# Kernel tuning notes

Hardware: AMD Instinct MI355X
Metric: run time of the kernel (lower is better)

The kernel has to match this reference:

```python
import jax, jax.numpy as jnp
import numpy as np

N = 100000
E = 1600000
IN_C, HID_C, OUT_C = 128, 128, 64


def setup_inputs() -> dict:
    key = jax.random.key(0)
    k = jax.random.split(key, 8)
    x = jax.random.normal(k[0], (N, IN_C), dtype=jnp.float32)
    edge_index = jax.random.randint(k[1], (2, E), 0, N, dtype=jnp.int64)
    edge_attr = jax.random.uniform(k[2], (E,), dtype=jnp.float32)
    # Glorot-ish init for GCNConv weights, zero bias (PyG default)
    W1 = jax.random.normal(k[3], (IN_C, HID_C), dtype=jnp.float32) / np.sqrt(IN_C)
    b1 = jnp.zeros((HID_C,), dtype=jnp.float32)
    W2 = jax.random.normal(k[4], (HID_C, OUT_C), dtype=jnp.float32) / np.sqrt(HID_C)
    b2 = jnp.zeros((OUT_C,), dtype=jnp.float32)
    return {"x": x, "edge_index": edge_index, "edge_attr": edge_attr,
            "W1": W1, "b1": b1, "W2": W2, "b2": b2}


def _gcn_conv(x, W, b, src, dst, ew):
    """PyG GCNConv: add self-loops (weight 1), symmetric normalization,
    aggregate x@W over edges src->dst, add bias."""
    n = x.shape[0]
    loop = jnp.arange(n, dtype=src.dtype)
    src_f = jnp.concatenate([src, loop])            # [E+N]
    dst_f = jnp.concatenate([dst, loop])
    ew_f = jnp.concatenate([ew, jnp.ones((n,), dtype=ew.dtype)])
    deg = jax.ops.segment_sum(ew_f, dst_f, num_segments=n)  # [N]
    dis = jnp.where(deg > 0, jax.lax.rsqrt(jnp.maximum(deg, 1e-12)), 0.0)
    norm = dis[src_f] * ew_f * dis[dst_f]           # [E+N]
    h = x @ W                                       # [N, C_out]
    msg = norm[:, None] * h[src_f]                  # [E+N, C_out] gather
    out = jax.ops.segment_sum(msg, dst_f, num_segments=n)   # scatter-add
    return out + b


def reference(x, edge_index, edge_attr, W1, b1, W2, b2):
    src, dst = edge_index[0], edge_index[1]
    h = _gcn_conv(x, W1, b1, src, dst, edge_attr)
    h = jax.nn.relu(h)
    # dropout is identity in eval mode (training=False)
    out = _gcn_conv(h, W2, b2, src, dst, edge_attr)
    return out
```

## Files before the change

### kernel.cpp

```cpp
#include <hip/hip_runtime.h>

#define NN 100000
#define EE 1600000
#define NBKT 391
#define NCHK 391
#define BINCHUNK 4096
#define CAP 5120

typedef unsigned int uint;
typedef unsigned short ushort;
typedef unsigned long long u64;

__device__ inline ushort f2bf(float f) {
    uint u = __float_as_uint(f);
    return (ushort)((u + 0x7fffu + ((u >> 16) & 1u)) >> 16);
}
__device__ inline float bf_lo(uint u) { return __uint_as_float(u << 16); }
__device__ inline float bf_hi(uint u) { return __uint_as_float(u & 0xffff0000u); }

__global__ __launch_bounds__(256) void k_count(const int* __restrict__ dst,
                                               int* __restrict__ gcount) {
    __shared__ int bh[NBKT];
    int t = threadIdx.x;
    for (int i = t; i < NBKT; i += 256) bh[i] = 0;
    __syncthreads();
    int base = blockIdx.x * BINCHUNK;
    int lim = min(EE - base, BINCHUNK);
    for (int i = t; i < lim; i += 256) atomicAdd(&bh[dst[base + i] >> 8], 1);
    __syncthreads();
    for (int i = t; i < NBKT; i += 256)
        if (bh[i]) atomicAdd(&gcount[i], bh[i]);
}

__global__ __launch_bounds__(512) void k_bscan(const int* __restrict__ gcount,
                                               int* __restrict__ bofs,
                                               int* __restrict__ gcursor,
                                               int* __restrict__ rowptr) {
    __shared__ int buf[2][512];
    int t = threadIdx.x;
    int v = (t < NBKT) ? gcount[t] : 0;
    int pi = 0;
    buf[0][t] = v;
    __syncthreads();
    for (int off = 1; off < 512; off <<= 1) {
        int po = pi ^ 1;
        int add = (t >= off) ? buf[pi][t - off] : 0;
        buf[po][t] = buf[pi][t] + add;
        __syncthreads();
        pi = po;
    }
    int excl = buf[pi][t] - v;
    if (t < NBKT) { bofs[t] = excl; gcursor[t] = excl; }
    if (t == 0) { bofs[NBKT] = EE; rowptr[NN] = EE; }
}

__global__ __launch_bounds__(256) void k_bin(const int* __restrict__ src,
                                             const int* __restrict__ dst,
                                             const float* __restrict__ ew,
                                             int* __restrict__ gcursor,
                                             u64* __restrict__ recs) {
    __shared__ int bh[NBKT], start[NBKT], lc[NBKT];
    int t = threadIdx.x;
    for (int i = t; i < NBKT; i += 256) { bh[i] = 0; lc[i] = 0; }
    __syncthreads();
    int base = blockIdx.x * BINCHUNK;
    int lim = min(EE - base, BINCHUNK);
    for (int i = t; i < lim; i += 256) atomicAdd(&bh[dst[base + i] >> 8], 1);
    __syncthreads();
    for (int i = t; i < NBKT; i += 256)
        if (bh[i]) start[i] = atomicAdd(&gcursor[i], bh[i]);
    __syncthreads();
    for (int i = t; i < lim; i += 256) {
        int e = base + i;
        int d = dst[e];
        int b = d >> 8;
        int r = atomicAdd(&lc[b], 1);
        recs[start[b] + r] = ((u64)__float_as_uint(ew[e]) << 25) |
                             ((u64)(uint)src[e] << 8) | (u64)(uint)(d & 255);
    }
}

__global__ __launch_bounds__(256) void k_sort(const u64* __restrict__ recs,
                                              const int* __restrict__ bofs,
                                              float* __restrict__ dis,
                                              int* __restrict__ rowptr,
                                              int2* __restrict__ epk) {
    __shared__ u64 rl[CAP];
    __shared__ int hist[256], cur[256];
    __shared__ float degf[256];
    __shared__ int sb[2][256];
    int t = threadIdx.x;
    int b = blockIdx.x;
    int base = bofs[b], cnt = bofs[b + 1] - base;
    hist[t] = 0; cur[t] = 0; degf[t] = 0.f;
    __syncthreads();
    for (int i = t; i < cnt; i += 256) {
        u64 r = recs[base + i];
        if (i < CAP) rl[i] = r;
        int dl = (int)(r & 255);
        atomicAdd(&hist[dl], 1);
        atomicAdd(&degf[dl], __uint_as_float((uint)(r >> 25)));
    }
    __syncthreads();
    int v = hist[t];
    int pi = 0;
    sb[0][t] = v;
    __syncthreads();
    for (int off = 1; off < 256; off <<= 1) {
        int po = pi ^ 1;
        int add = (t >= off) ? sb[pi][t - off] : 0;
        sb[po][t] = sb[pi][t] + add;
        __syncthreads();
        pi = po;
    }
    int lofs = sb[pi][t] - v;
    int node = (b << 8) + t;
    if (node < NN) {
        dis[node] = rsqrtf(1.0f + degf[t]);
        rowptr[node] = base + lofs;
    }
    hist[t] = lofs;
    __syncthreads();
    for (int i = t; i < cnt; i += 256) {
        u64 r = (i < CAP) ? rl[i] : recs[base + i];
        int dl = (int)(r & 255);
        int pos = hist[dl] + atomicAdd(&cur[dl], 1);
        epk[base + pos] = make_int2((int)((r >> 8) & 0x1FFFF), (int)(uint)(r >> 25));
    }
}

__global__ __launch_bounds__(256) void k_gemm1(const float* __restrict__ x,
                                               const float* __restrict__ W,
                                               ushort* __restrict__ h) {
    __shared__ float Wl[128 * 128];
    __shared__ float xt[128 * 32];
    int t = threadIdx.x;
    int rb = blockIdx.x * 32;

    const float4* W4 = (const float4*)W;
    float4* Wl4 = (float4*)Wl;
#pragma unroll
    for (int i = 0; i < 16; i++) Wl4[t + 256 * i] = W4[t + 256 * i];

#pragma unroll
    for (int i = 0; i < 4; i++) {
        int idx = t + 256 * i;
        int r = idx >> 5;
        int c4 = idx & 31;
        float4 v = ((const float4*)(x + (size_t)(rb + r) * 128))[c4];
        int kc = c4 << 2;
        xt[(kc + 0) * 32 + r] = v.x;
        xt[(kc + 1) * 32 + r] = v.y;
        xt[(kc + 2) * 32 + r] = v.z;
        xt[(kc + 3) * 32 + r] = v.w;
    }
    __syncthreads();

    int tc = t & 31;
    int tr = t >> 5;
    float acc[4][4] = {};
#pragma unroll 4
    for (int k = 0; k < 128; k++) {
        float4 wv = ((const float4*)(Wl + k * 128))[tc];
        float4 xv = ((const float4*)(xt + k * 32))[tr];
        float xs[4] = {xv.x, xv.y, xv.z, xv.w};
        float ws[4] = {wv.x, wv.y, wv.z, wv.w};
#pragma unroll
        for (int r = 0; r < 4; r++)
#pragma unroll
            for (int c = 0; c < 4; c++) acc[r][c] += xs[r] * ws[c];
    }
#pragma unroll
    for (int r = 0; r < 4; r++) {
        int row = rb + tr * 4 + r;
        ushort4 o = {f2bf(acc[r][0]), f2bf(acc[r][1]), f2bf(acc[r][2]), f2bf(acc[r][3])};
        ((ushort4*)(h + (size_t)row * 128))[tc] = o;
    }
}

__global__ __launch_bounds__(256) void k_gemm2(const float* __restrict__ a,
                                               const float* __restrict__ W,
                                               ushort* __restrict__ h) {
    __shared__ float Wl[128 * 64];
    __shared__ float at[128 * 64];
    int t = threadIdx.x;
    int rb = blockIdx.x * 64;

    const float4* W4 = (const float4*)W;
    float4* Wl4 = (float4*)Wl;
#pragma unroll
    for (int i = 0; i < 8; i++) Wl4[t + 256 * i] = W4[t + 256 * i];

#pragma unroll
    for (int i = 0; i < 8; i++) {
        int idx = t + 256 * i;
        int r = idx >> 5;
        int c4 = idx & 31;
        int row = rb + r;
        if (row >= NN) row = NN - 1;
        float4 v = ((const float4*)(a + (size_t)row * 128))[c4];
        int kc = c4 << 2;
        at[(kc + 0) * 64 + r] = v.x;
        at[(kc + 1) * 64 + r] = v.y;
        at[(kc + 2) * 64 + r] = v.z;
        at[(kc + 3) * 64 + r] = v.w;
    }
    __syncthreads();

    int tc = t & 15;
    int tr = t >> 4;
    float acc[4][4] = {};
#pragma unroll 4
    for (int k = 0; k < 128; k++) {
        float4 wv = ((const float4*)(Wl + k * 64))[tc];
        float4 av = ((const float4*)(at + k * 64))[tr];
        float as[4] = {av.x, av.y, av.z, av.w};
        float ws[4] = {wv.x, wv.y, wv.z, wv.w};
#pragma unroll
        for (int r = 0; r < 4; r++)
#pragma unroll
            for (int c = 0; c < 4; c++) acc[r][c] += as[r] * ws[c];
    }
#pragma unroll
    for (int r = 0; r < 4; r++) {
        int row = rb + tr * 4 + r;
        if (row < NN) {
            ushort4 o = {f2bf(acc[r][0]), f2bf(acc[r][1]), f2bf(acc[r][2]), f2bf(acc[r][3])};
            ((ushort4*)(h + (size_t)row * 64))[tc] = o;
        }
    }
}

__global__ __launch_bounds__(256) void k_agg1(const int* __restrict__ rowptr,
                                              const int2* __restrict__ epk,
                                              const float* __restrict__ dis,
                                              const ushort* __restrict__ h,
                                              const float* __restrict__ b,
                                              float* __restrict__ a) {
    int wid = (blockIdx.x * blockDim.x + threadIdx.x) >> 6;
    int lane = threadIdx.x & 63;
    if (wid >= NN) return;
    int beg = rowptr[wid], end = rowptr[wid + 1];
    const uint* hp = (const uint*)h;
    uint us = hp[(size_t)wid * 64 + lane];
    float di = dis[wid];
    float2 bv = ((const float2*)b)[lane];

    float2 acc0 = {0.f, 0.f}, acc1 = {0.f, 0.f};
    float2 acc2 = {0.f, 0.f}, acc3 = {0.f, 0.f};
    int j = beg;
    for (; j + 3 < end; j += 4) {
        int2 p0 = epk[j];
        int2 p1 = epk[j + 1];
        int2 p2 = epk[j + 2];
        int2 p3 = epk[j + 3];
        uint u0 = hp[(size_t)p0.x * 64 + lane];
        uint u1 = hp[(size_t)p1.x * 64 + lane];
        uint u2 = hp[(size_t)p2.x * 64 + lane];
        uint u3 = hp[(size_t)p3.x * 64 + lane];
        float w0 = dis[p0.x] * __int_as_float(p0.y);
        float w1 = dis[p1.x] * __int_as_float(p1.y);
        float w2 = dis[p2.x] * __int_as_float(p2.y);
        float w3 = dis[p3.x] * __int_as_float(p3.y);
        acc0.x += w0 * bf_lo(u0); acc0.y += w0 * bf_hi(u0);
        acc1.x += w1 * bf_lo(u1); acc1.y += w1 * bf_hi(u1);
        acc2.x += w2 * bf_lo(u2); acc2.y += w2 * bf_hi(u2);
        acc3.x += w3 * bf_lo(u3); acc3.y += w3 * bf_hi(u3);
    }
    for (; j < end; j++) {
        int2 p0 = epk[j];
        float w0 = dis[p0.x] * __int_as_float(p0.y);
        uint u0 = hp[(size_t)p0.x * 64 + lane];
        acc0.x += w0 * bf_lo(u0); acc0.y += w0 * bf_hi(u0);
    }
    float sx = (acc0.x + acc1.x) + (acc2.x + acc3.x);
    float sy = (acc0.y + acc1.y) + (acc2.y + acc3.y);
    float ox = di * sx + di * di * bf_lo(us) + bv.x;
    float oy = di * sy + di * di * bf_hi(us) + bv.y;
    float2 o = {fmaxf(ox, 0.f), fmaxf(oy, 0.f)};
    ((float2*)a)[(size_t)wid * 64 + lane] = o;
}

__global__ __launch_bounds__(256) void k_agg2(const int* __restrict__ rowptr,
                                              const int2* __restrict__ epk,
                                              const float* __restrict__ dis,
                                              const ushort* __restrict__ h,
                                              const float* __restrict__ b,
                                              float* __restrict__ out) {
    int wid = (blockIdx.x * blockDim.x + threadIdx.x) >> 6;
    int lane = threadIdx.x & 63;
    if (wid >= NN) return;
    int beg = rowptr[wid], end = rowptr[wid + 1];
    float hv = __uint_as_float(((uint)h[(size_t)wid * 64 + lane]) << 16);
    float di = dis[wid];
    float bl = b[lane];

    float acc0 = 0.f, acc1 = 0.f, acc2 = 0.f, acc3 = 0.f;
    int j = beg;
    for (; j + 3 < end; j += 4) {
        int2 p0 = epk[j];
        int2 p1 = epk[j + 1];
        int2 p2 = epk[j + 2];
        int2 p3 = epk[j + 3];
        float v0 = __uint_as_float(((uint)h[(size_t)p0.x * 64 + lane]) << 16);
        float v1 = __uint_as_float(((uint)h[(size_t)p1.x * 64 + lane]) << 16);
        float v2 = __uint_as_float(((uint)h[(size_t)p2.x * 64 + lane]) << 16);
        float v3 = __uint_as_float(((uint)h[(size_t)p3.x * 64 + lane]) << 16);
        acc0 += dis[p0.x] * __int_as_float(p0.y) * v0;
        acc1 += dis[p1.x] * __int_as_float(p1.y) * v1;
        acc2 += dis[p2.x] * __int_as_float(p2.y) * v2;
        acc3 += dis[p3.x] * __int_as_float(p3.y) * v3;
    }
    for (; j < end; j++) {
        int2 p0 = epk[j];
        acc0 += dis[p0.x] * __int_as_float(p0.y) *
                __uint_as_float(((uint)h[(size_t)p0.x * 64 + lane]) << 16);
    }
    float s = (acc0 + acc1) + (acc2 + acc3);
    out[(size_t)wid * 64 + lane] = di * s + di * di * hv + bl;
}

extern "C" void kernel_launch(void* const* d_in, const int* in_sizes, int n_in,
                              void* d_out, int out_size, void* d_ws, size_t ws_size,
                              hipStream_t stream) {
    const float* x  = (const float*)d_in[0];
    const int* ei   = (const int*)d_in[1];
    const float* ew = (const float*)d_in[2];
    const float* W1 = (const float*)d_in[3];
    const float* b1 = (const float*)d_in[4];
    const float* W2 = (const float*)d_in[5];
    const float* b2 = (const float*)d_in[6];
    float* out      = (float*)d_out;

    const int* src = ei;
    const int* dst = ei + EE;

    int* gcount  = (int*)d_ws;
    int* bofs    = gcount + 512;
    int* gcursor = bofs + 512;
    float* dis   = (float*)(gcursor + 512);
    int* rowptr  = (int*)(dis + 100000);
    u64* recs    = (u64*)(rowptr + 100002);
    int2* epk    = (int2*)recs;
    ushort* hb   = (ushort*)(recs + EE);
    float* a1    = (float*)(hb + (size_t)NN * 128);

    hipMemsetAsync(gcount, 0, 512 * sizeof(int), stream);
    k_count<<<NCHK, 256, 0, stream>>>(dst, gcount);
    k_bscan<<<1, 512, 0, stream>>>(gcount, bofs, gcursor, rowptr);
    k_bin<<<NCHK, 256, 0, stream>>>(src, dst, ew, gcursor, recs);
    k_sort<<<NBKT, 256, 0, stream>>>(recs, bofs, dis, rowptr, epk);

    k_gemm1<<<NN / 32, 256, 0, stream>>>(x, W1, hb);
    k_agg1<<<(NN * 64 + 255) / 256, 256, 0, stream>>>(rowptr, epk, dis, hb, b1, a1);

    k_gemm2<<<(NN + 63) / 64, 256, 0, stream>>>(a1, W2, hb);
    k_agg2<<<(NN * 64 + 255) / 256, 256, 0, stream>>>(rowptr, epk, dis, hb, b2, out);
}
```

Baseline: 467.7 us.

## Premultiply edge weights by source norm, store hidden layer as bf16, deepen gather batching

Adds a pass that folds dis[src] into each packed edge weight once, so both aggregation kernels drop the per-edge random dis lookup. The first aggregation now writes its ReLU output in bf16 and the second GEMM reads bf16, halving that intermediate's traffic. The aggregation loops issue 16 edge loads and then 16 feature gathers per batch, with masked tails, to raise memory-level parallelism. The cost is an extra kernel over all edges, more registers per thread, and extra bf16 rounding of the hidden activations.

Result: no change. 467.3 us (-0.1%).

```diff
diff --git a/kernel.cpp b/kernel.cpp
--- a/kernel.cpp
+++ b/kernel.cpp
@@ -17,6 +17,7 @@
 }
 __device__ inline float bf_lo(uint u) { return __uint_as_float(u << 16); }
 __device__ inline float bf_hi(uint u) { return __uint_as_float(u & 0xffff0000u); }
+__device__ inline float bf2f(ushort s) { return __uint_as_float((uint)s << 16); }
 
 __global__ __launch_bounds__(256) void k_count(const int* __restrict__ dst,
                                                int* __restrict__ gcount) {
@@ -127,6 +128,15 @@
         int pos = hist[dl] + atomicAdd(&cur[dl], 1);
         epk[base + pos] = make_int2((int)((r >> 8) & 0x1FFFF), (int)(uint)(r >> 25));
     }
+}
+
+__global__ __launch_bounds__(256) void k_wmul(int2* __restrict__ epk,
+                                              const float* __restrict__ dis) {
+    int e = blockIdx.x * blockDim.x + threadIdx.x;
+    if (e >= EE) return;
+    int2 p = epk[e];
+    float w = dis[p.x] * __int_as_float(p.y);
+    epk[e] = make_int2(p.x, __float_as_int(w));
 }
 
 __global__ __launch_bounds__(256) void k_gemm1(const float* __restrict__ x,
@@ -178,11 +188,11 @@
     }
 }
 
-__global__ __launch_bounds__(256) void k_gemm2(const float* __restrict__ a,
+__global__ __launch_bounds__(256) void k_gemm2(const ushort* __restrict__ a,
                                                const float* __restrict__ W,
                                                ushort* __restrict__ h) {
     __shared__ float Wl[128 * 64];
-    __shared__ float at[128 * 64];
+    __shared__ ushort at[128 * 64];
     int t = threadIdx.x;
     int rb = blockIdx.x * 64;
 
@@ -192,18 +202,22 @@
     for (int i = 0; i < 8; i++) Wl4[t + 256 * i] = W4[t + 256 * i];
 
 #pragma unroll
-    for (int i = 0; i < 8; i++) {
+    for (int i = 0; i < 4; i++) {
         int idx = t + 256 * i;
-        int r = idx >> 5;
-        int c4 = idx & 31;
+        int r = idx >> 4;
+        int c8 = idx & 15;
         int row = rb + r;
         if (row >= NN) row = NN - 1;
-        float4 v = ((const float4*)(a + (size_t)row * 128))[c4];
-        int kc = c4 << 2;
-        at[(kc + 0) * 64 + r] = v.x;
-        at[(kc + 1) * 64 + r] = v.y;
-        at[(kc + 2) * 64 + r] = v.z;
-        at[(kc + 3) * 64 + r] = v.w;
+        uint4 u = ((const uint4*)(a + (size_t)row * 128))[c8];
+        int kc = c8 << 3;
+        at[(kc + 0) * 64 + r] = (ushort)(u.x & 0xffffu);
+        at[(kc + 1) * 64 + r] = (ushort)(u.x >> 16);
+        at[(kc + 2) * 64 + r] = (ushort)(u.y & 0xffffu);
+        at[(kc + 3) * 64 + r] = (ushort)(u.y >> 16);
+        at[(kc + 4) * 64 + r] = (ushort)(u.z & 0xffffu);
+        at[(kc + 5) * 64 + r] = (ushort)(u.z >> 16);
+        at[(kc + 6) * 64 + r] = (ushort)(u.w & 0xffffu);
+        at[(kc + 7) * 64 + r] = (ushort)(u.w >> 16);
     }
     __syncthreads();
 
@@ -213,8 +227,8 @@
 #pragma unroll 4
     for (int k = 0; k < 128; k++) {
         float4 wv = ((const float4*)(Wl + k * 64))[tc];
-        float4 av = ((const float4*)(at + k * 64))[tr];
-        float as[4] = {av.x, av.y, av.z, av.w};
+        ushort4 av = *(const ushort4*)(at + k * 64 + tr * 4);
+        float as[4] = {bf2f(av.x), bf2f(av.y), bf2f(av.z), bf2f(av.w)};
         float ws[4] = {wv.x, wv.y, wv.z, wv.w};
 #pragma unroll
         for (int r = 0; r < 4; r++)
@@ -236,7 +250,7 @@
                                               const float* __restrict__ dis,
                                               const ushort* __restrict__ h,
                                               const float* __restrict__ b,
-                                              float* __restrict__ a) {
+                                              ushort* __restrict__ a) {
     int wid = (blockIdx.x * blockDim.x + threadIdx.x) >> 6;
     int lane = threadIdx.x & 63;
     if (wid >= NN) return;
@@ -248,37 +262,32 @@
 
     float2 acc0 = {0.f, 0.f}, acc1 = {0.f, 0.f};
     float2 acc2 = {0.f, 0.f}, acc3 = {0.f, 0.f};
-    int j = beg;
-    for (; j + 3 < end; j += 4) {
-        int2 p0 = epk[j];
-        int2 p1 = epk[j + 1];
-        int2 p2 = epk[j + 2];
-        int2 p3 = epk[j + 3];
-        uint u0 = hp[(size_t)p0.x * 64 + lane];
-        uint u1 = hp[(size_t)p1.x * 64 + lane];
-        uint u2 = hp[(size_t)p2.x * 64 + lane];
-        uint u3 = hp[(size_t)p3.x * 64 + lane];
-        float w0 = dis[p0.x] * __int_as_float(p0.y);
-        float w1 = dis[p1.x] * __int_as_float(p1.y);
-        float w2 = dis[p2.x] * __int_as_float(p2.y);
-        float w3 = dis[p3.x] * __int_as_float(p3.y);
-        acc0.x += w0 * bf_lo(u0); acc0.y += w0 * bf_hi(u0);
-        acc1.x += w1 * bf_lo(u1); acc1.y += w1 * bf_hi(u1);
-        acc2.x += w2 * bf_lo(u2); acc2.y += w2 * bf_hi(u2);
-        acc3.x += w3 * bf_lo(u3); acc3.y += w3 * bf_hi(u3);
-    }
-    for (; j < end; j++) {
-        int2 p0 = epk[j];
-        float w0 = dis[p0.x] * __int_as_float(p0.y);
-        uint u0 = hp[(size_t)p0.x * 64 + lane];
-        acc0.x += w0 * bf_lo(u0); acc0.y += w0 * bf_hi(u0);
+    for (int j = beg; j < end; j += 16) {
+        int ps[16]; float ww[16]; uint uu[16];
+#pragma unroll
+        for (int k = 0; k < 16; k++) {
+            int idx = j + k;
+            bool vld = idx < end;
+            int2 p = epk[vld ? idx : end - 1];
+            ps[k] = p.x;
+            ww[k] = vld ? __int_as_float(p.y) : 0.f;
+        }
+#pragma unroll
+        for (int k = 0; k < 16; k++) uu[k] = hp[(size_t)ps[k] * 64 + lane];
+#pragma unroll
+        for (int k = 0; k < 16; k++) {
+            float2* A = (k & 3) == 0 ? &acc0 : (k & 3) == 1 ? &acc1
+                       : (k & 3) == 2 ? &acc2 : &acc3;
+            A->x += ww[k] * bf_lo(uu[k]);
+            A->y += ww[k] * bf_hi(uu[k]);
+        }
     }
     float sx = (acc0.x + acc1.x) + (acc2.x + acc3.x);
     float sy = (acc0.y + acc1.y) + (acc2.y + acc3.y);
     float ox = di * sx + di * di * bf_lo(us) + bv.x;
     float oy = di * sy + di * di * bf_hi(us) + bv.y;
-    float2 o = {fmaxf(ox, 0.f), fmaxf(oy, 0.f)};
-    ((float2*)a)[(size_t)wid * 64 + lane] = o;
+    ushort2 o = {f2bf(fmaxf(ox, 0.f)), f2bf(fmaxf(oy, 0.f))};
+    ((ushort2*)a)[(size_t)wid * 64 + lane] = o;
 }
 
 __global__ __launch_bounds__(256) void k_agg2(const int* __restrict__ rowptr,
@@ -291,30 +300,31 @@
     int lane = threadIdx.x & 63;
     if (wid >= NN) return;
     int beg = rowptr[wid], end = rowptr[wid + 1];
-    float hv = __uint_as_float(((uint)h[(size_t)wid * 64 + lane]) << 16);
+    float hv = bf2f(h[(size_t)wid * 64 + lane]);
     float di = dis[wid];
     float bl = b[lane];
 
     float acc0 = 0.f, acc1 = 0.f, acc2 = 0.f, acc3 = 0.f;
-    int j = beg;
-    for (; j + 3 < end; j += 4) {
-        int2 p0 = epk[j];
-        int2 p1 = epk[j + 1];
-        int2 p2 = epk[j + 2];
-        int2 p3 = epk[j + 3];
-        float v0 = __uint_as_float(((uint)h[(size_t)p0.x * 64 + lane]) << 16);
-        float v1 = __uint_as_float(((uint)h[(size_t)p1.x * 64 + lane]) << 16);
-        float v2 = __uint_as_float(((uint)h[(size_t)p2.x * 64 + lane]) << 16);
-        float v3 = __uint_as_float(((uint)h[(size_t)p3.x * 64 + lane]) << 16);
-        acc0 += dis[p0.x] * __int_as_float(p0.y) * v0;
-        acc1 += dis[p1.x] * __int_as_float(p1.y) * v1;
-        acc2 += dis[p2.x] * __int_as_float(p2.y) * v2;
-        acc3 += dis[p3.x] * __int_as_float(p3.y) * v3;
-    }
-    for (; j < end; j++) {
-        int2 p0 = epk[j];
-        acc0 += dis[p0.x] * __int_as_float(p0.y) *
-                __uint_as_float(((uint)h[(size_t)p0.x * 64 + lane]) << 16);
+    for (int j = beg; j < end; j += 16) {
+        int ps[16]; float ww[16]; ushort vv[16];
+#pragma unroll
+        for (int k = 0; k < 16; k++) {
+            int idx = j + k;
+            bool vld = idx < end;
+            int2 p = epk[vld ? idx : end - 1];
+            ps[k] = p.x;
+            ww[k] = vld ? __int_as_float(p.y) : 0.f;
+        }
+#pragma unroll
+        for (int k = 0; k < 16; k++) vv[k] = h[(size_t)ps[k] * 64 + lane];
+#pragma unroll
+        for (int k = 0; k < 16; k++) {
+            float val = ww[k] * bf2f(vv[k]);
+            if ((k & 3) == 0) acc0 += val;
+            else if ((k & 3) == 1) acc1 += val;
+            else if ((k & 3) == 2) acc2 += val;
+            else acc3 += val;
+        }
     }
     float s = (acc0 + acc1) + (acc2 + acc3);
     out[(size_t)wid * 64 + lane] = di * s + di * di * hv + bl;
@@ -343,13 +353,14 @@
     u64* recs    = (u64*)(rowptr + 100002);
     int2* epk    = (int2*)recs;
     ushort* hb   = (ushort*)(recs + EE);
-    float* a1    = (float*)(hb + (size_t)NN * 128);
+    ushort* a1   = hb + (size_t)NN * 128;
 
     hipMemsetAsync(gcount, 0, 512 * sizeof(int), stream);
     k_count<<<NCHK, 256, 0, stream>>>(dst, gcount);
     k_bscan<<<1, 512, 0, stream>>>(gcount, bofs, gcursor, rowptr);
     k_bin<<<NCHK, 256, 0, stream>>>(src, dst, ew, gcursor, recs);
     k_sort<<<NBKT, 256, 0, stream>>>(recs, bofs, dis, rowptr, epk);
+    k_wmul<<<(EE + 255) / 256, 256, 0, stream>>>(epk, dis);
 
     k_gemm1<<<NN / 32, 256, 0, stream>>>(x, W1, hb);
     k_agg1<<<(NN * 64 + 255) / 256, 256, 0, stream>>>(rowptr, epk, dis, hb, b1, a1);
```
